# Optimization experiments

Measured on AMD Instinct MI355X. Metric: run time of the kernel, lower is better.

The kernel has to match this reference:

```python
import jax, jax.numpy as jnp
import numpy as np

DT = 0.1  # time step (forward arg dt in the torch module)


def setup_inputs() -> dict:
    key = jax.random.key(0)
    k1, k2, k3, k4 = jax.random.split(key, 4)
    B, T = 256, 100_000
    # Pre-generated 3-state Markov trajectory (the torch module generates this
    # on the host with sequential RNG; here it is a fixed int input).
    states = jax.random.randint(k1, (B, T), 0, 3).astype(jnp.int32)
    # Unit orientation vectors; entry k is the heading after the k-th tumble.
    e0s = jax.random.normal(k2, (B, T + 1, 3), dtype=jnp.float32)
    e0s = e0s / jnp.linalg.norm(e0s, axis=-1, keepdims=True)
    speed_0 = jax.random.uniform(k3, (B,), dtype=jnp.float32) * 0.001
    speed_1 = jax.random.uniform(k4, (B,), dtype=jnp.float32) * 0.005
    x0 = jnp.zeros((B, 3), jnp.float32)
    return {"states": states, "e0s": e0s, "speed_0": speed_0,
            "speed_1": speed_1, "x0": x0}


def reference(states, e0s, speed_0, speed_1, x0):
    """Vectorized equivalent of simulate_particle_trajectory (pauses=0 path).

    The per-particle while-loop with run-length segments reduces, when
    nonp_pause_type is None (pauses == 0), to:
      e0_exp[b, t] = 0                                  if states[b,t] == 2
                   = e0s[b, k(b,t)] * speed_{s}[b]       otherwise,
    where k(b,t) = number of tumbles (state==2) at steps <= t (inclusive
    cumsum: at a tumble step the output is zeroed anyway, and the step after
    the k-th tumble uses orientation e0s[k], matching the loop's k counter).
    Positions integrate the velocity: x[t] = x0 + dt * cumsum(e0_exp).
    """
    is_tumble = states == 2                                   # (B, T)
    k = jnp.cumsum(is_tumble.astype(jnp.int32), axis=1)        # (B, T)
    e0_sel = jnp.take_along_axis(e0s, k[:, :, None], axis=1)   # (B, T, 3) gather
    speed = jnp.where(states == 0, speed_0[:, None], speed_1[:, None])  # (B, T)
    vel = e0_sel * jnp.where(is_tumble, 0.0, speed)[..., None]  # e0_exp
    X = x0[:, None, :] + jnp.cumsum(vel, axis=1) * jnp.float32(DT)
    return X
```

## Files before the change

### kernel.cpp

```cpp
#include <hip/hip_runtime.h>


#define NT    1024
#define IPT   8
#define CHUNK (NT * IPT)
#define NW    (NT / 64)
#define SLOT  25

__global__ __launch_bounds__(NT)
void traj_kernel(const int*   __restrict__ states,
                 const float* __restrict__ e0s,
                 const float* __restrict__ sp0v,
                 const float* __restrict__ sp1v,
                 const float* __restrict__ x0,
                 float*       __restrict__ X,
                 int T)
{
    const int b    = blockIdx.x;
    const int tid  = threadIdx.x;
    const int lane = tid & 63;
    const int wid  = tid >> 6;

    __shared__ float s_out[NT * SLOT];
    __shared__ int   s_wi[NW];
    __shared__ float s_wf[NW][3];

    const int*   st = states + (size_t)b * T;
    const float* er = e0s    + (size_t)b * (T + 1) * 3;
    float*       xr = X      + (size_t)b * T * 3;
    const float sp0 = sp0v[b], sp1 = sp1v[b];
    const float x00 = x0[3 * b + 0], x01 = x0[3 * b + 1], x02 = x0[3 * b + 2];

    int   kc  = 0;
    float pcx = 0.f, pcy = 0.f, pcz = 0.f;

    for (int base = 0; base < T; base += CHUNK) {
        int my[IPT];
        const int e0i = base + tid * IPT;
        if (e0i + IPT <= T) {
            int4 a = *(const int4*)(st + e0i);
            int4 c4 = *(const int4*)(st + e0i + 4);
            my[0] = a.x;  my[1] = a.y;  my[2] = a.z;  my[3] = a.w;
            my[4] = c4.x; my[5] = c4.y; my[6] = c4.z; my[7] = c4.w;
        } else {
            #pragma unroll
            for (int j = 0; j < IPT; ++j)
                my[j] = (e0i + j < T) ? st[e0i + j] : 3;
        }

        int c = 0;
        #pragma unroll
        for (int j = 0; j < IPT; ++j) c += (my[j] == 2);
        int incl = c;
        #pragma unroll
        for (int d = 1; d < 64; d <<= 1) {
            int n = __shfl_up(incl, d, 64);
            if (lane >= d) incl += n;
        }
        if (lane == 63) s_wi[wid] = incl;
        __syncthreads();
        int wex = 0, btot = 0;
        #pragma unroll
        for (int w = 0; w < NW; ++w) {
            int t = s_wi[w];
            wex  += (w < wid) ? t : 0;
            btot += t;
        }
        int k = kc + wex + (incl - c);

        float plx[IPT], ply[IPT], plz[IPT];
        float px = 0.f, py = 0.f, pz = 0.f;
        #pragma unroll
        for (int j = 0; j < IPT; ++j) {
            const int s = my[j];
            k += (s == 2);
            const float sp = (s == 0) ? sp0 : ((s == 1) ? sp1 : 0.f);
            const float* e = er + (size_t)k * 3;
            px += e[0] * sp;
            py += e[1] * sp;
            pz += e[2] * sp;
            plx[j] = px; ply[j] = py; plz[j] = pz;
        }

        float ix = px, iy = py, iz = pz;
        #pragma unroll
        for (int d = 1; d < 64; d <<= 1) {
            float nx = __shfl_up(ix, d, 64);
            float ny = __shfl_up(iy, d, 64);
            float nz = __shfl_up(iz, d, 64);
            if (lane >= d) { ix += nx; iy += ny; iz += nz; }
        }
        if (lane == 63) { s_wf[wid][0] = ix; s_wf[wid][1] = iy; s_wf[wid][2] = iz; }
        __syncthreads();
        float wfx = 0.f, wfy = 0.f, wfz = 0.f, btx = 0.f, bty = 0.f, btz = 0.f;
        #pragma unroll
        for (int w = 0; w < NW; ++w) {
            float tx = s_wf[w][0], ty = s_wf[w][1], tz = s_wf[w][2];
            if (w < wid) { wfx += tx; wfy += ty; wfz += tz; }
            btx += tx; bty += ty; btz += tz;
        }
        const float bx = pcx + wfx + (ix - px);
        const float by = pcy + wfy + (iy - py);
        const float bz = pcz + wfz + (iz - pz);

        float* o = s_out + tid * SLOT;
        #pragma unroll
        for (int j = 0; j < IPT; ++j) {
            o[3 * j + 0] = x00 + (bx + plx[j]) * 0.1f;
            o[3 * j + 1] = x01 + (by + ply[j]) * 0.1f;
            o[3 * j + 2] = x02 + (bz + plz[j]) * 0.1f;
        }
        __syncthreads();

        const int rem = T - base;
        const int cnt = rem < CHUNK ? rem : CHUNK;
        float* dst = xr + (size_t)base * 3;
        if (cnt == CHUNK) {
            #pragma unroll
            for (int j = 0; j < IPT * 3; ++j) {
                const int f = tid + j * NT;
                dst[f] = s_out[f + f / 24];
            }
        } else {
            const int nfl = cnt * 3;
            for (int f = tid; f < nfl; f += NT)
                dst[f] = s_out[f + f / 24];
        }

        kc  += btot;
        pcx += btx; pcy += bty; pcz += btz;
    }
}

extern "C" void kernel_launch(void* const* d_in, const int* in_sizes, int n_in,
                              void* d_out, int out_size, void* d_ws, size_t ws_size,
                              hipStream_t stream) {
    const int*   states = (const int*)  d_in[0];
    const float* e0s    = (const float*)d_in[1];
    const float* sp0    = (const float*)d_in[2];
    const float* sp1    = (const float*)d_in[3];
    const float* x0     = (const float*)d_in[4];
    float*       X      = (float*)d_out;

    const int B = in_sizes[2];
    const int T = in_sizes[0] / B;

    traj_kernel<<<dim3(B), dim3(NT), 0, stream>>>(states, e0s, sp0, sp1, x0, X, T);
}
```

Before: 622.5 us.

## Prefetch next chunk states and store outputs directly as float4 without LDS staging

Removes the 100KB shared-memory output staging buffer and its barrier, writing each thread's 24 contiguous floats directly with six float4 stores. Software-prefetches the next chunk's states into registers to overlap load latency with the scans. Splits the gather loop from the prefix accumulation so all e0s loads can be issued before the dependent adds. Direct stores are per-thread strided (96 bytes apart), so write coalescing is worse, but freeing LDS may allow more blocks per CU.

New measurement: 594.2 us. 1.05x faster.

```diff
diff --git a/kernel.cpp b/kernel.cpp
--- a/kernel.cpp
+++ b/kernel.cpp
@@ -5,7 +5,20 @@
 #define IPT   8
 #define CHUNK (NT * IPT)
 #define NW    (NT / 64)
-#define SLOT  25
+
+__device__ __forceinline__ void load_states(const int* __restrict__ st, int T,
+                                            int e0i, int out[IPT]) {
+    if (e0i + IPT <= T) {
+        int4 a = *(const int4*)(st + e0i);
+        int4 b = *(const int4*)(st + e0i + 4);
+        out[0] = a.x; out[1] = a.y; out[2] = a.z; out[3] = a.w;
+        out[4] = b.x; out[5] = b.y; out[6] = b.z; out[7] = b.w;
+    } else {
+        #pragma unroll
+        for (int j = 0; j < IPT; ++j)
+            out[j] = (e0i + j < T) ? st[e0i + j] : 3;
+    }
+}
 
 __global__ __launch_bounds__(NT)
 void traj_kernel(const int*   __restrict__ states,
@@ -21,7 +34,6 @@
     const int lane = tid & 63;
     const int wid  = tid >> 6;
 
-    __shared__ float s_out[NT * SLOT];
     __shared__ int   s_wi[NW];
     __shared__ float s_wf[NW][3];
 
@@ -34,23 +46,17 @@
     int   kc  = 0;
     float pcx = 0.f, pcy = 0.f, pcz = 0.f;
 
+    int cur[IPT];
+    load_states(st, T, tid * IPT, cur);
+
     for (int base = 0; base < T; base += CHUNK) {
-        int my[IPT];
-        const int e0i = base + tid * IPT;
-        if (e0i + IPT <= T) {
-            int4 a = *(const int4*)(st + e0i);
-            int4 c4 = *(const int4*)(st + e0i + 4);
-            my[0] = a.x;  my[1] = a.y;  my[2] = a.z;  my[3] = a.w;
-            my[4] = c4.x; my[5] = c4.y; my[6] = c4.z; my[7] = c4.w;
-        } else {
-            #pragma unroll
-            for (int j = 0; j < IPT; ++j)
-                my[j] = (e0i + j < T) ? st[e0i + j] : 3;
-        }
+        int nxt[IPT];
+        const bool has_next = (base + CHUNK) < T;
+        if (has_next) load_states(st, T, base + CHUNK + tid * IPT, nxt);
 
         int c = 0;
         #pragma unroll
-        for (int j = 0; j < IPT; ++j) c += (my[j] == 2);
+        for (int j = 0; j < IPT; ++j) c += (cur[j] == 2);
         int incl = c;
         #pragma unroll
         for (int d = 1; d < 64; d <<= 1) {
@@ -68,18 +74,24 @@
         }
         int k = kc + wex + (incl - c);
 
-        float plx[IPT], ply[IPT], plz[IPT];
+        float ex[IPT], ey[IPT], ez[IPT];
+        #pragma unroll
+        for (int j = 0; j < IPT; ++j) {
+            const int s = cur[j];
+            k += (s == 2);
+            const float sp = (s == 0) ? sp0 : ((s == 1) ? sp1 : 0.f);
+            const float* e = er + (size_t)k * 3;
+            ex[j] = e[0] * sp;
+            ey[j] = e[1] * sp;
+            ez[j] = e[2] * sp;
+        }
+
+        float o[IPT * 3];
         float px = 0.f, py = 0.f, pz = 0.f;
         #pragma unroll
         for (int j = 0; j < IPT; ++j) {
-            const int s = my[j];
-            k += (s == 2);
-            const float sp = (s == 0) ? sp0 : ((s == 1) ? sp1 : 0.f);
-            const float* e = er + (size_t)k * 3;
-            px += e[0] * sp;
-            py += e[1] * sp;
-            pz += e[2] * sp;
-            plx[j] = px; ply[j] = py; plz[j] = pz;
+            px += ex[j]; py += ey[j]; pz += ez[j];
+            o[3 * j + 0] = px; o[3 * j + 1] = py; o[3 * j + 2] = pz;
         }
 
         float ix = px, iy = py, iz = pz;
@@ -103,32 +115,35 @@
         const float by = pcy + wfy + (iy - py);
         const float bz = pcz + wfz + (iz - pz);
 
-        float* o = s_out + tid * SLOT;
         #pragma unroll
         for (int j = 0; j < IPT; ++j) {
-            o[3 * j + 0] = x00 + (bx + plx[j]) * 0.1f;
-            o[3 * j + 1] = x01 + (by + ply[j]) * 0.1f;
-            o[3 * j + 2] = x02 + (bz + plz[j]) * 0.1f;
+            o[3 * j + 0] = x00 + (bx + o[3 * j + 0]) * 0.1f;
+            o[3 * j + 1] = x01 + (by + o[3 * j + 1]) * 0.1f;
+            o[3 * j + 2] = x02 + (bz + o[3 * j + 2]) * 0.1f;
         }
-        __syncthreads();
-
-        const int rem = T - base;
-        const int cnt = rem < CHUNK ? rem : CHUNK;
-        float* dst = xr + (size_t)base * 3;
-        if (cnt == CHUNK) {
+        const int e0i = base + tid * IPT;
+        if (e0i + IPT <= T) {
+            float4* d4 = (float4*)(xr + (size_t)e0i * 3);
+            d4[0] = make_float4(o[0],  o[1],  o[2],  o[3]);
+            d4[1] = make_float4(o[4],  o[5],  o[6],  o[7]);
+            d4[2] = make_float4(o[8],  o[9],  o[10], o[11]);
+            d4[3] = make_float4(o[12], o[13], o[14], o[15]);
+            d4[4] = make_float4(o[16], o[17], o[18], o[19]);
+            d4[5] = make_float4(o[20], o[21], o[22], o[23]);
+        } else {
             #pragma unroll
-            for (int j = 0; j < IPT * 3; ++j) {
-                const int f = tid + j * NT;
-                dst[f] = s_out[f + f / 24];
-            }
-        } else {
-            const int nfl = cnt * 3;
-            for (int f = tid; f < nfl; f += NT)
-                dst[f] = s_out[f + f / 24];
+            for (int j = 0; j < IPT; ++j)
+                if (e0i + j < T) {
+                    float* d = xr + (size_t)(e0i + j) * 3;
+                    d[0] = o[3 * j + 0]; d[1] = o[3 * j + 1]; d[2] = o[3 * j + 2];
+                }
         }
 
         kc  += btot;
         pcx += btx; pcy += bty; pcz += btz;
+
+        #pragma unroll
+        for (int j = 0; j < IPT; ++j) cur[j] = nxt[j];
     }
 }
 
```
